# Performance work log

Measured on AMD Instinct MI355X. Metric: run time of the kernel, lower is better.

## Reference

```python
import jax, jax.numpy as jnp
import numpy as np

N = 50000        # nodes
E = 800000       # edges (avg degree 16)
F_IN = 128       # num_node_features
HEADS = 4        # const.NUM_HEADS
CH = 32          # const.NUM_CHANNELS
CLS = 40         # num_classes
NEG_SLOPE = 0.2  # PyG GATv2Conv default


def setup_inputs() -> dict:
    key = jax.random.key(0)
    ks = jax.random.split(key, 10)
    x = jax.random.normal(ks[0], (N, F_IN), dtype=jnp.float32)
    edge_index = jax.random.randint(ks[1], (2, E), 0, N, dtype=jnp.int64)
    s1 = 1.0 / np.sqrt(F_IN)
    s2 = 1.0 / np.sqrt(HEADS * CH)
    w1_l = jax.random.normal(ks[2], (F_IN, HEADS * CH), jnp.float32) * s1
    w1_r = jax.random.normal(ks[3], (F_IN, HEADS * CH), jnp.float32) * s1
    a1 = jax.random.normal(ks[4], (HEADS, CH), jnp.float32) * (1.0 / np.sqrt(CH))
    b1 = jnp.zeros((HEADS * CH,), jnp.float32)
    w2_l = jax.random.normal(ks[5], (HEADS * CH, CLS), jnp.float32) * s2
    w2_r = jax.random.normal(ks[6], (HEADS * CH, CLS), jnp.float32) * s2
    a2 = jax.random.normal(ks[7], (1, CLS), jnp.float32) * (1.0 / np.sqrt(CLS))
    b2 = jnp.zeros((CLS,), jnp.float32)
    return {"x": x, "edge_index": edge_index, "w1_l": w1_l, "w1_r": w1_r,
            "a1": a1, "b1": b1, "w2_l": w2_l, "w2_r": w2_r, "a2": a2, "b2": b2}


def _gatv2_conv(x, src, dst, wl, wr, a, b, concat):
    """GATv2Conv (PyG semantics, eval mode: no dropout).
    src -> lin_l, dst -> lin_r; e = a . LeakyReLU(x_l[src] + x_r[dst]);
    segment softmax over dst; out_i = sum_j alpha * x_l[src]."""
    H, C = a.shape
    n = x.shape[0]
    xl = (x @ wl).reshape(n, H, C)
    xr = (x @ wr).reshape(n, H, C)
    # per-edge additive attention logits [E, H]
    e = jnp.einsum('ehc,hc->eh', jax.nn.leaky_relu(xl[src] + xr[dst], NEG_SLOPE), a)
    # numerically stable segment softmax over target nodes
    m = jax.ops.segment_max(e, dst, num_segments=n)          # [n, H]
    p = jnp.exp(e - m[dst])
    denom = jax.ops.segment_sum(p, dst, num_segments=n)     # [n, H]
    alpha = p / denom[dst]
    out = jax.ops.segment_sum(alpha[..., None] * xl[src], dst, num_segments=n)  # [n, H, C]
    out = out.reshape(n, H * C) if concat else out.mean(axis=1)
    return out + b


def reference(x, edge_index, w1_l, w1_r, a1, b1, w2_l, w2_r, a2, b2):
    n = x.shape[0]
    # PyG GATv2Conv default add_self_loops=True
    loop = jnp.arange(n, dtype=edge_index.dtype)
    src = jnp.concatenate([edge_index[0], loop])
    dst = jnp.concatenate([edge_index[1], loop])
    h = jax.nn.elu(_gatv2_conv(x, src, dst, w1_l, w1_r, a1, b1, concat=True))
    # F.dropout with training=False is identity
    out = _gatv2_conv(h, src, dst, w2_l, w2_r, a2, b2, concat=False)
    return jax.nn.log_softmax(out, axis=1)
```

## Files before the change

### kernel.cpp

```cpp
#include <hip/hip_runtime.h>
#include <hip/hip_bf16.h>
#include <math.h>

#define NN 50000
#define NE 800000
#define ETOT (NE + NN)
#define CLS 40
#define CLSP 48
#define NEG 0.2f
#define MTILES (NN / 16)
#define GB1 ((MTILES + 3) / 4)
#define PREPB 176
#define NBUCK 196
#define BCAP 8192
#define EB 4096
#define KAB ((ETOT + EB - 1) / EB)

typedef __hip_bfloat16 bf16;
typedef __attribute__((ext_vector_type(8))) __bf16 bf16x8;
typedef __attribute__((ext_vector_type(4))) float f32x4;
struct U3 { unsigned x, y, z; };

__device__ __forceinline__ bf16x8 cvt8(f32x4 a, f32x4 b) {
    bf16x8 r;
    r[0] = (__bf16)a[0]; r[1] = (__bf16)a[1]; r[2] = (__bf16)a[2]; r[3] = (__bf16)a[3];
    r[4] = (__bf16)b[0]; r[5] = (__bf16)b[1]; r[6] = (__bf16)b[2]; r[7] = (__bf16)b[3];
    return r;
}
__device__ __forceinline__ void unpk(unsigned u, float& lo, float& hi) {
    lo = __uint_as_float(u << 16);
    hi = __uint_as_float(u & 0xffff0000u);
}
__device__ __forceinline__ void unpk8(uint4 u, float* x) {
    unpk(u.x, x[0], x[1]); unpk(u.y, x[2], x[3]);
    unpk(u.z, x[4], x[5]); unpk(u.w, x[6], x[7]);
}
__device__ __forceinline__ void unpk6(U3 u, float* x) {
    unpk(u.x, x[0], x[1]); unpk(u.y, x[2], x[3]); unpk(u.z, x[4], x[5]);
}
__device__ __forceinline__ float leaky(float v) { return fmaxf(v, NEG * v); }

__device__ __forceinline__ unsigned scan256(unsigned v, unsigned* wsum) {
    int t = threadIdx.x;
    int lane = t & 63, w = t >> 6;
    unsigned inc = v;
#pragma unroll
    for (int d = 1; d < 64; d <<= 1) {
        unsigned x = __shfl_up(inc, d);
        if (lane >= d) inc += x;
    }
    if (lane == 63) wsum[w] = inc;
    __syncthreads();
    unsigned woff = 0;
#pragma unroll
    for (int i = 0; i < 4; i++) woff += (i < w) ? wsum[i] : 0;
    return woff + inc - v;
}

__global__ __launch_bounds__(256) void prep(
        const float* __restrict__ w1l, const float* __restrict__ w1r,
        const float* __restrict__ w2l, const float* __restrict__ w2r,
        bf16* __restrict__ wT1, bf16* __restrict__ wT2,
        int* __restrict__ bcursor) {
    int t = blockIdx.x * 256 + threadIdx.x;
    if (t < NBUCK) bcursor[t] = 0;
    if (t < 2 * 128 * 128) {
        int m = t >> 14;
        int idx = t & 16383;
        int n = idx >> 7, k = idx & 127;
        const float* w = m ? w1r : w1l;
        wT1[t] = __float2bfloat16(w[k * 128 + n]);
    } else if (t < 2 * 128 * 128 + 2 * CLSP * 128) {
        int u = t - 2 * 128 * 128;
        int m = u / (CLSP * 128);
        int idx = u % (CLSP * 128);
        int n = idx >> 7, k = idx & 127;
        const float* w = m ? w2r : w2l;
        wT2[u] = __float2bfloat16((n < CLS) ? w[k * CLS + n] : 0.0f);
    }
}

__global__ __launch_bounds__(256) void gemm1_scatter(
        const float* __restrict__ x, const bf16* __restrict__ wT,
        bf16* __restrict__ outL, bf16* __restrict__ outR,
        const int* __restrict__ ei, int* __restrict__ bcursor,
        uint2* __restrict__ tmp) {
    __shared__ unsigned hist[256];
    __shared__ unsigned lstart[256];
    __shared__ unsigned lcur[256];
    __shared__ unsigned gbase[256];
    __shared__ unsigned wsum[4];
    __shared__ uint2 binned[EB];
    __shared__ unsigned target[EB];
    if ((int)blockIdx.x < GB1) {
        int wave = threadIdx.x >> 6;
        int lane = threadIdx.x & 63;
        int tile = blockIdx.x * 4 + wave;
        if (tile >= MTILES) return;
        const bf16* wl = wT;
        const bf16* wr = wT + 128 * 128;
        int row0 = tile * 16;
        int l16 = lane & 15, quad = lane >> 4;
        f32x4 z = {0.f, 0.f, 0.f, 0.f};
        f32x4 accl[8], accr[8];
#pragma unroll
        for (int i = 0; i < 8; i++) { accl[i] = z; accr[i] = z; }
        const float* xrow = x + (size_t)(row0 + l16) * 128 + quad * 8;
#pragma unroll
        for (int k0 = 0; k0 < 128; k0 += 32) {
            f32x4 a0 = *reinterpret_cast<const f32x4*>(xrow + k0);
            f32x4 a1v = *reinterpret_cast<const f32x4*>(xrow + k0 + 4);
            bf16x8 a = cvt8(a0, a1v);
#pragma unroll
            for (int ct = 0; ct < 8; ct++) {
                bf16x8 bl = *reinterpret_cast<const bf16x8*>(wl + (ct * 16 + l16) * 128 + k0 + quad * 8);
                bf16x8 br = *reinterpret_cast<const bf16x8*>(wr + (ct * 16 + l16) * 128 + k0 + quad * 8);
                accl[ct] = __builtin_amdgcn_mfma_f32_16x16x32_bf16(a, bl, accl[ct], 0, 0, 0);
                accr[ct] = __builtin_amdgcn_mfma_f32_16x16x32_bf16(a, br, accr[ct], 0, 0, 0);
            }
        }
#pragma unroll
        for (int ct = 0; ct < 8; ct++)
#pragma unroll
            for (int r = 0; r < 4; r++) {
                size_t o = (size_t)(row0 + quad * 4 + r) * 128 + ct * 16 + l16;
                outL[o] = __float2bfloat16(accl[ct][r]);
                outR[o] = __float2bfloat16(accr[ct][r]);
            }
    } else {
        int t = threadIdx.x;
        int e0 = (blockIdx.x - GB1) * EB;
        hist[t] = 0;
        __syncthreads();
        int srcs[16], dsts[16];
#pragma unroll
        for (int i = 0; i < 16; i++) {
            int e = e0 + i * 256 + t;
            if (e < ETOT) {
                int s, d;
                if (e < NE) { s = ei[e]; d = ei[NE + e]; }
                else        { s = d = e - NE; }
                srcs[i] = s; dsts[i] = d;
                atomicAdd(&hist[d >> 8], 1u);
            } else dsts[i] = -1;
        }
        __syncthreads();
        unsigned v = hist[t];
        unsigned excl = scan256(v, wsum);
        lstart[t] = excl;
        lcur[t] = 0;
        __syncthreads();
        if (t < NBUCK && v > 0)
            gbase[t] = (unsigned)atomicAdd(&bcursor[t], (int)v) + (unsigned)t * BCAP;
        __syncthreads();
#pragma unroll
        for (int i = 0; i < 16; i++) {
            int d = dsts[i];
            if (d >= 0) {
                int bk = d >> 8;
                unsigned p = atomicAdd(&lcur[bk], 1u);
                unsigned slot = lstart[bk] + p;
                binned[slot] = make_uint2((unsigned)srcs[i], (unsigned)d);
                target[slot] = gbase[bk] + p;
            }
        }
        __syncthreads();
        int tot = min(EB, ETOT - e0);
        for (int s = t; s < tot; s += 256)
            tmp[target[s]] = binned[s];
    }
}

__global__ __launch_bounds__(256) void bucket_sort(const int* __restrict__ bcursor,
                                                   const uint2* __restrict__ tmp,
                                                   int* __restrict__ csr_src,
                                                   int* __restrict__ startA,
                                                   int* __restrict__ degA) {
    __shared__ unsigned hist[256];
    __shared__ unsigned lcur[256];
    __shared__ unsigned wsum[4];
    int b = blockIdx.x, t = threadIdx.x;
    int cnt = bcursor[b];
    hist[t] = 0;
    __syncthreads();
    const uint2* seg = tmp + (size_t)b * BCAP;
    for (int s = t; s < cnt; s += 256)
        atomicAdd(&hist[seg[s].y & 255], 1u);
    __syncthreads();
    unsigned v = hist[t];
    unsigned excl = scan256(v, wsum);
    lcur[t] = excl;
    int node = b * 256 + t;
    if (node < NN) {
        startA[node] = b * BCAP + (int)excl;
        degA[node] = (int)v;
    }
    __syncthreads();
    int* cbase = csr_src + (size_t)b * BCAP;
    for (int s = t; s < cnt; s += 256) {
        uint2 p = seg[s];
        unsigned pos = atomicAdd(&lcur[p.y & 255], 1u);
        cbase[pos] = (int)p.x;
    }
}

struct L1S { float s; float acc[8]; };
__device__ __forceinline__ void l1_consume(uint4 u, bool valid, const float* xrf,
                                           const float* a1f, L1S& st) {
    float x[8];
    unpk8(u, x);
    float e = 0.f;
#pragma unroll
    for (int k = 0; k < 8; k++) e += a1f[k] * leaky(x[k] + xrf[k]);
    e += __shfl_xor(e, 1);
    e += __shfl_xor(e, 2);
    float w = valid ? __expf(e) : 0.f;
    st.s += w;
#pragma unroll
    for (int k = 0; k < 8; k++) st.acc[k] += w * x[k];
}

__global__ __launch_bounds__(256) void node_l1(const int* __restrict__ startA,
                                               const int* __restrict__ degA,
                                               const int* __restrict__ csr_src,
                                               const bf16* __restrict__ xl,
                                               const bf16* __restrict__ xr,
                                               const float* __restrict__ a1,
                                               const float* __restrict__ b1,
                                               bf16* __restrict__ hb) {
    int wid = (blockIdx.x * 256 + threadIdx.x) >> 6;
    int lane = threadIdx.x & 63;
    int g = lane >> 4, t = lane & 15;
    unsigned cB = (unsigned)t * 16;
    int j0 = startA[wid];
    int deg = degA[wid];
    unsigned rowB = (unsigned)csr_src[j0 + min(lane, deg - 1)] << 8;
    const char* xlb = (const char*)xl;
    float xrf[8];
    unpk8(*(const uint4*)((const char*)xr + ((unsigned)wid << 8) + cB), xrf);
    float a1f[8];
    {
        f32x4 lo = *reinterpret_cast<const f32x4*>(a1 + t * 8);
        f32x4 hi = *reinterpret_cast<const f32x4*>(a1 + t * 8 + 4);
#pragma unroll
        for (int k = 0; k < 4; k++) { a1f[k] = lo[k]; a1f[k + 4] = hi[k]; }
    }
    L1S st; st.s = 0.f;
#pragma unroll
    for (int k = 0; k < 8; k++) st.acc[k] = 0.f;
    int lim = min(deg, 64);
    int nb = (deg + 3) >> 2;
    int b = 0;
    for (; (b + 4) * 4 <= lim; b += 4) {
        unsigned o0 = __shfl(rowB, b * 4 + g) + cB;
        unsigned o1 = __shfl(rowB, b * 4 + 4 + g) + cB;
        unsigned o2 = __shfl(rowB, b * 4 + 8 + g) + cB;
        unsigned o3 = __shfl(rowB, b * 4 + 12 + g) + cB;
        uint4 u0 = *(const uint4*)(xlb + o0);
        uint4 u1 = *(const uint4*)(xlb + o1);
        uint4 u2 = *(const uint4*)(xlb + o2);
        uint4 u3 = *(const uint4*)(xlb + o3);
        l1_consume(u0, true, xrf, a1f, st);
        l1_consume(u1, true, xrf, a1f, st);
        l1_consume(u2, true, xrf, a1f, st);
        l1_consume(u3, true, xrf, a1f, st);
    }
    for (; (b + 2) * 4 <= lim; b += 2) {
        unsigned o0 = __shfl(rowB, b * 4 + g) + cB;
        unsigned o1 = __shfl(rowB, b * 4 + 4 + g) + cB;
        uint4 u0 = *(const uint4*)(xlb + o0);
        uint4 u1 = *(const uint4*)(xlb + o1);
        l1_consume(u0, true, xrf, a1f, st);
        l1_consume(u1, true, xrf, a1f, st);
    }
    for (; b < nb; b++) {
        int p = b * 4 + g;
        bool valid = p < deg;
        int pp = valid ? p : deg - 1;
        unsigned o = __shfl(rowB, min(pp, 63)) + cB;
        if (pp >= 64) o = (((unsigned)csr_src[j0 + pp]) << 8) + cB;
        uint4 u = *(const uint4*)(xlb + o);
        l1_consume(u, valid, xrf, a1f, st);
    }
#pragma unroll
    for (int d = 16; d < 64; d <<= 1) {
        st.s += __shfl_xor(st.s, d);
#pragma unroll
        for (int k = 0; k < 8; k++) st.acc[k] += __shfl_xor(st.acc[k], d);
    }
    if (g == 0) {
        float inv = 1.f / st.s;
        unsigned pk[4];
#pragma unroll
        for (int k = 0; k < 4; k++) {
            float o0 = st.acc[2 * k] * inv + b1[t * 8 + 2 * k];
            float o1 = st.acc[2 * k + 1] * inv + b1[t * 8 + 2 * k + 1];
            o0 = o0 > 0.f ? o0 : __expf(o0) - 1.f;
            o1 = o1 > 0.f ? o1 : __expf(o1) - 1.f;
            bf16 r0 = __float2bfloat16(o0), r1 = __float2bfloat16(o1);
            pk[k] = (unsigned)*reinterpret_cast<unsigned short*>(&r0) |
                    ((unsigned)*reinterpret_cast<unsigned short*>(&r1) << 16);
        }
        uint4 w4 = {pk[0], pk[1], pk[2], pk[3]};
        *(uint4*)((char*)hb + ((unsigned)wid << 8) + cB) = w4;
    }
}

__global__ __launch_bounds__(256) void gemm2(const bf16* __restrict__ h,
                                             const bf16* __restrict__ wT,
                                             bf16* __restrict__ outL,
                                             bf16* __restrict__ outR) {
    int wave = threadIdx.x >> 6;
    int lane = threadIdx.x & 63;
    int tile = blockIdx.x * 4 + wave;
    if (tile >= MTILES) return;
    const bf16* wl = wT;
    const bf16* wr = wT + CLSP * 128;
    int row0 = tile * 16;
    int l16 = lane & 15, quad = lane >> 4;
    f32x4 z = {0.f, 0.f, 0.f, 0.f};
    f32x4 accl[3], accr[3];
#pragma unroll
    for (int i = 0; i < 3; i++) { accl[i] = z; accr[i] = z; }
    const bf16* hrow = h + (size_t)(row0 + l16) * 128 + quad * 8;
#pragma unroll
    for (int k0 = 0; k0 < 128; k0 += 32) {
        bf16x8 a = *reinterpret_cast<const bf16x8*>(hrow + k0);
#pragma unroll
        for (int ct = 0; ct < 3; ct++) {
            bf16x8 bl = *reinterpret_cast<const bf16x8*>(wl + (ct * 16 + l16) * 128 + k0 + quad * 8);
            bf16x8 br = *reinterpret_cast<const bf16x8*>(wr + (ct * 16 + l16) * 128 + k0 + quad * 8);
            accl[ct] = __builtin_amdgcn_mfma_f32_16x16x32_bf16(a, bl, accl[ct], 0, 0, 0);
            accr[ct] = __builtin_amdgcn_mfma_f32_16x16x32_bf16(a, br, accr[ct], 0, 0, 0);
        }
    }
#pragma unroll
    for (int ct = 0; ct < 3; ct++)
#pragma unroll
        for (int r = 0; r < 4; r++) {
            size_t o = (size_t)(row0 + quad * 4 + r) * CLSP + ct * 16 + l16;
            outL[o] = __float2bfloat16(accl[ct][r]);
            outR[o] = __float2bfloat16(accr[ct][r]);
        }
}

struct L2S { float s; float acc[6]; };
__device__ __forceinline__ void l2_consume(U3 u, bool valid, const float* xrf,
                                           const float* a2f, L2S& st) {
    float x[6];
    unpk6(u, x);
    float e = 0.f;
#pragma unroll
    for (int k = 0; k < 6; k++) e += a2f[k] * leaky(x[k] + xrf[k]);
    e += __shfl_xor(e, 1);
    e += __shfl_xor(e, 2);
    e += __shfl_xor(e, 4);
    float w = valid ? __expf(e) : 0.f;
    st.s += w;
#pragma unroll
    for (int k = 0; k < 6; k++) st.acc[k] += w * x[k];
}

__global__ __launch_bounds__(256) void node_l2(const int* __restrict__ startA,
                                               const int* __restrict__ degA,
                                               const int* __restrict__ csr_src,
                                               const bf16* __restrict__ xl2,
                                               const bf16* __restrict__ xr2,
                                               const float* __restrict__ a2,
                                               const float* __restrict__ b2,
                                               float* __restrict__ out) {
    int wid = (blockIdx.x * 256 + threadIdx.x) >> 6;
    int lane = threadIdx.x & 63;
    int g = lane >> 3, t = lane & 7;
    unsigned cB = (unsigned)t * 12;
    int j0 = startA[wid];
    int deg = degA[wid];
    unsigned rowB = (unsigned)csr_src[j0 + min(lane, deg - 1)] * 96u;
    const char* xlb = (const char*)xl2;
    float xrf[6];
    unpk6(*(const U3*)((const char*)xr2 + (unsigned)wid * 96u + cB), xrf);
    int c = t * 6;
    float a2f[6];
#pragma unroll
    for (int k = 0; k < 6; k++) a2f[k] = (c + k < CLS) ? a2[c + k] : 0.f;
    L2S st; st.s = 0.f;
#pragma unroll
    for (int k = 0; k < 6; k++) st.acc[k] = 0.f;
    int lim = min(deg, 64);
    int nb = (deg + 7) >> 3;
    int b = 0;
    for (; (b + 2) * 8 <= lim; b += 2) {
        unsigned o0 = __shfl(rowB, b * 8 + g) + cB;
        unsigned o1 = __shfl(rowB, b * 8 + 8 + g) + cB;
        U3 u0 = *(const U3*)(xlb + o0);
        U3 u1 = *(const U3*)(xlb + o1);
        l2_consume(u0, true, xrf, a2f, st);
        l2_consume(u1, true, xrf, a2f, st);
    }
    for (; b < nb; b++) {
        int p = b * 8 + g;
        bool valid = p < deg;
        int pp = valid ? p : deg - 1;
        unsigned o = __shfl(rowB, min(pp, 63)) + cB;
        if (pp >= 64) o = (unsigned)csr_src[j0 + pp] * 96u + cB;
        U3 u = *(const U3*)(xlb + o);
        l2_consume(u, valid, xrf, a2f, st);
    }
#pragma unroll
    for (int d = 8; d < 64; d <<= 1) {
        st.s += __shfl_xor(st.s, d);
#pragma unroll
        for (int k = 0; k < 6; k++) st.acc[k] += __shfl_xor(st.acc[k], d);
    }
    float inv = 1.f / st.s;
    float q[6];
    float mx = -3e38f;
#pragma unroll
    for (int k = 0; k < 6; k++) {
        bool val = (c + k < CLS);
        q[k] = val ? (st.acc[k] * inv + b2[c + k]) : -3e38f;
        mx = fmaxf(mx, q[k]);
    }
    mx = fmaxf(mx, __shfl_xor(mx, 1));
    mx = fmaxf(mx, __shfl_xor(mx, 2));
    mx = fmaxf(mx, __shfl_xor(mx, 4));
    float se = 0.f;
#pragma unroll
    for (int k = 0; k < 6; k++) if (c + k < CLS) se += __expf(q[k] - mx);
    se += __shfl_xor(se, 1);
    se += __shfl_xor(se, 2);
    se += __shfl_xor(se, 4);
    float ls = mx + __logf(se);
    if (g == 0) {
        float* o = out + (size_t)wid * CLS + c;
#pragma unroll
        for (int k = 0; k < 6; k++)
            if (c + k < CLS) o[k] = q[k] - ls;
    }
}

extern "C" void kernel_launch(void* const* d_in, const int* in_sizes, int n_in,
                              void* d_out, int out_size, void* d_ws, size_t ws_size,
                              hipStream_t stream) {
    const float* x   = (const float*)d_in[0];
    const int*   ei  = (const int*)d_in[1];
    const float* w1l = (const float*)d_in[2];
    const float* w1r = (const float*)d_in[3];
    const float* a1  = (const float*)d_in[4];
    const float* b1  = (const float*)d_in[5];
    const float* w2l = (const float*)d_in[6];
    const float* w2r = (const float*)d_in[7];
    const float* a2  = (const float*)d_in[8];
    const float* b2  = (const float*)d_in[9];
    float* out = (float*)d_out;

    char* base = (char*)d_ws;
    int*   bcursor = (int*)(base + 0);
    int*   startA  = (int*)(base + 1024);
    int*   degA    = (int*)(base + 201024);
    uint2* tmp     = (uint2*)(base + 401024);
    int*   csr_src = (int*)(base + 13246080);
    bf16*  xl1     = (bf16*)(base + 19668608);
    bf16*  hb      = (bf16*)(base + 45268608);
    bf16*  xl2p    = (bf16*)(base + 58068608);
    bf16*  wT1     = (bf16*)(base + 67668608);
    bf16*  wT2     = (bf16*)(base + 67734144);
    bf16* xr1  = xl1 + (size_t)NN * 128;
    bf16* xr2p = xl2p + (size_t)NN * CLSP;

    prep<<<PREPB, 256, 0, stream>>>(w1l, w1r, w2l, w2r, wT1, wT2, bcursor);
    gemm1_scatter<<<GB1 + KAB, 256, 0, stream>>>(x, wT1, xl1, xr1, ei, bcursor, tmp);
    bucket_sort<<<NBUCK, 256, 0, stream>>>(bcursor, tmp, csr_src, startA, degA);
    node_l1<<<(NN * 64) / 256, 256, 0, stream>>>(startA, degA, csr_src, xl1, xr1, a1, b1, hb);
    gemm2<<<GB1, 256, 0, stream>>>(hb, wT2, xl2p, xr2p);
    node_l2<<<(NN * 64) / 256, 256, 0, stream>>>(startA, degA, csr_src, xl2p, xr2p, a2, b2, out);
}
```

Baseline: 237.8 us.

## Sort nodes by degree within buckets and vectorize per-edge math as float2

bucket_sort now builds a per-bucket permutation of nodes grouped by in-degree (counting sort over 64 degree classes). node_l1 and node_l2 map each wavefront to a permuted node, so waves in a block have similar trip counts and less load imbalance. Padding entries past NN exit early. The per-edge attention and accumulation math is also rewritten on float2 vectors to encourage packed FP32 instructions. The cost is scattered node order for the xr/hb/out accesses and an extra perm read per wave.

Result: slower. 243.8 us (+2.5%).

```diff
diff --git a/kernel.cpp b/kernel.cpp
--- a/kernel.cpp
+++ b/kernel.cpp
@@ -15,10 +15,13 @@
 #define BCAP 8192
 #define EB 4096
 #define KAB ((ETOT + EB - 1) / EB)
+#define PERMN (NBUCK * 256)
+#define NODEB (PERMN / 4)
 
 typedef __hip_bfloat16 bf16;
 typedef __attribute__((ext_vector_type(8))) __bf16 bf16x8;
 typedef __attribute__((ext_vector_type(4))) float f32x4;
+typedef __attribute__((ext_vector_type(2))) float f32x2;
 struct U3 { unsigned x, y, z; };
 
 __device__ __forceinline__ bf16x8 cvt8(f32x4 a, f32x4 b) {
@@ -27,18 +30,19 @@
     r[4] = (__bf16)b[0]; r[5] = (__bf16)b[1]; r[6] = (__bf16)b[2]; r[7] = (__bf16)b[3];
     return r;
 }
-__device__ __forceinline__ void unpk(unsigned u, float& lo, float& hi) {
-    lo = __uint_as_float(u << 16);
-    hi = __uint_as_float(u & 0xffff0000u);
-}
-__device__ __forceinline__ void unpk8(uint4 u, float* x) {
-    unpk(u.x, x[0], x[1]); unpk(u.y, x[2], x[3]);
-    unpk(u.z, x[4], x[5]); unpk(u.w, x[6], x[7]);
-}
-__device__ __forceinline__ void unpk6(U3 u, float* x) {
-    unpk(u.x, x[0], x[1]); unpk(u.y, x[2], x[3]); unpk(u.z, x[4], x[5]);
-}
-__device__ __forceinline__ float leaky(float v) { return fmaxf(v, NEG * v); }
+__device__ __forceinline__ f32x2 unpk2(unsigned u) {
+    f32x2 r;
+    r.x = __uint_as_float(u << 16);
+    r.y = __uint_as_float(u & 0xffff0000u);
+    return r;
+}
+__device__ __forceinline__ f32x2 leaky2(f32x2 v) {
+    f32x2 s = v * NEG;
+    f32x2 r;
+    r.x = fmaxf(v.x, s.x);
+    r.y = fmaxf(v.y, s.y);
+    return r;
+}
 
 __device__ __forceinline__ unsigned scan256(unsigned v, unsigned* wsum) {
     int t = threadIdx.x;
@@ -175,13 +179,17 @@
                                                    const uint2* __restrict__ tmp,
                                                    int* __restrict__ csr_src,
                                                    int* __restrict__ startA,
-                                                   int* __restrict__ degA) {
+                                                   int* __restrict__ degA,
+                                                   unsigned* __restrict__ perm) {
     __shared__ unsigned hist[256];
     __shared__ unsigned lcur[256];
     __shared__ unsigned wsum[4];
+    __shared__ unsigned dbase[64];
+    __shared__ unsigned dcur[64];
     int b = blockIdx.x, t = threadIdx.x;
     int cnt = bcursor[b];
     hist[t] = 0;
+    if (t < 64) dcur[t] = 0;
     __syncthreads();
     const uint2* seg = tmp + (size_t)b * BCAP;
     for (int s = t; s < cnt; s += 256)
@@ -191,11 +199,28 @@
     unsigned excl = scan256(v, wsum);
     lcur[t] = excl;
     int node = b * 256 + t;
-    if (node < NN) {
+    bool real = node < NN;
+    if (real) {
         startA[node] = b * BCAP + (int)excl;
         degA[node] = (int)v;
     }
+    unsigned dc = real ? min(v, 62u) : 63u;
+    atomicAdd(&dcur[dc], 1u);
     __syncthreads();
+    if (t < 64) {
+        unsigned bv = dcur[t];
+        unsigned inc = bv;
+#pragma unroll
+        for (int d = 1; d < 64; d <<= 1) {
+            unsigned xx = __shfl_up(inc, d);
+            if ((t & 63) >= d) inc += xx;
+        }
+        dbase[t] = inc - bv;
+        dcur[t] = 0;
+    }
+    __syncthreads();
+    unsigned rank = dbase[dc] + atomicAdd(&dcur[dc], 1u);
+    perm[b * 256 + rank] = (unsigned)node;
     int* cbase = csr_src + (size_t)b * BCAP;
     for (int s = t; s < cnt; s += 256) {
         uint2 p = seg[s];
@@ -204,23 +229,25 @@
     }
 }
 
-struct L1S { float s; float acc[8]; };
-__device__ __forceinline__ void l1_consume(uint4 u, bool valid, const float* xrf,
-                                           const float* a1f, L1S& st) {
-    float x[8];
-    unpk8(u, x);
-    float e = 0.f;
-#pragma unroll
-    for (int k = 0; k < 8; k++) e += a1f[k] * leaky(x[k] + xrf[k]);
+struct L1S { float s; f32x2 acc[4]; };
+__device__ __forceinline__ void l1_consume(uint4 u, bool valid, const f32x2* xrf,
+                                           const f32x2* a1f, L1S& st) {
+    f32x2 x0 = unpk2(u.x), x1 = unpk2(u.y), x2 = unpk2(u.z), x3 = unpk2(u.w);
+    f32x2 e2 = a1f[0] * leaky2(x0 + xrf[0]);
+    e2 += a1f[1] * leaky2(x1 + xrf[1]);
+    e2 += a1f[2] * leaky2(x2 + xrf[2]);
+    e2 += a1f[3] * leaky2(x3 + xrf[3]);
+    float e = e2.x + e2.y;
     e += __shfl_xor(e, 1);
     e += __shfl_xor(e, 2);
     float w = valid ? __expf(e) : 0.f;
     st.s += w;
-#pragma unroll
-    for (int k = 0; k < 8; k++) st.acc[k] += w * x[k];
-}
-
-__global__ __launch_bounds__(256) void node_l1(const int* __restrict__ startA,
+    st.acc[0] += w * x0; st.acc[1] += w * x1;
+    st.acc[2] += w * x2; st.acc[3] += w * x3;
+}
+
+__global__ __launch_bounds__(256) void node_l1(const unsigned* __restrict__ perm,
+                                               const int* __restrict__ startA,
                                                const int* __restrict__ degA,
                                                const int* __restrict__ csr_src,
                                                const bf16* __restrict__ xl,
@@ -229,25 +256,27 @@
                                                const float* __restrict__ b1,
                                                bf16* __restrict__ hb) {
     int wid = (blockIdx.x * 256 + threadIdx.x) >> 6;
+    unsigned nid = perm[wid];
+    if (nid >= NN) return;
     int lane = threadIdx.x & 63;
     int g = lane >> 4, t = lane & 15;
     unsigned cB = (unsigned)t * 16;
-    int j0 = startA[wid];
-    int deg = degA[wid];
+    int j0 = startA[nid];
+    int deg = degA[nid];
     unsigned rowB = (unsigned)csr_src[j0 + min(lane, deg - 1)] << 8;
     const char* xlb = (const char*)xl;
-    float xrf[8];
-    unpk8(*(const uint4*)((const char*)xr + ((unsigned)wid << 8) + cB), xrf);
-    float a1f[8];
+    uint4 xru = *(const uint4*)((const char*)xr + (nid << 8) + cB);
+    f32x2 xrf[4] = {unpk2(xru.x), unpk2(xru.y), unpk2(xru.z), unpk2(xru.w)};
+    f32x2 a1f[4];
     {
         f32x4 lo = *reinterpret_cast<const f32x4*>(a1 + t * 8);
         f32x4 hi = *reinterpret_cast<const f32x4*>(a1 + t * 8 + 4);
-#pragma unroll
-        for (int k = 0; k < 4; k++) { a1f[k] = lo[k]; a1f[k + 4] = hi[k]; }
+        a1f[0].x = lo[0]; a1f[0].y = lo[1]; a1f[1].x = lo[2]; a1f[1].y = lo[3];
+        a1f[2].x = hi[0]; a1f[2].y = hi[1]; a1f[3].x = hi[2]; a1f[3].y = hi[3];
     }
     L1S st; st.s = 0.f;
 #pragma unroll
-    for (int k = 0; k < 8; k++) st.acc[k] = 0.f;
+    for (int k = 0; k < 4; k++) st.acc[k] = (f32x2){0.f, 0.f};
     int lim = min(deg, 64);
     int nb = (deg + 3) >> 2;
     int b = 0;
@@ -286,15 +315,18 @@
     for (int d = 16; d < 64; d <<= 1) {
         st.s += __shfl_xor(st.s, d);
 #pragma unroll
-        for (int k = 0; k < 8; k++) st.acc[k] += __shfl_xor(st.acc[k], d);
+        for (int k = 0; k < 4; k++) {
+            st.acc[k].x += __shfl_xor(st.acc[k].x, d);
+            st.acc[k].y += __shfl_xor(st.acc[k].y, d);
+        }
     }
     if (g == 0) {
         float inv = 1.f / st.s;
         unsigned pk[4];
 #pragma unroll
         for (int k = 0; k < 4; k++) {
-            float o0 = st.acc[2 * k] * inv + b1[t * 8 + 2 * k];
-            float o1 = st.acc[2 * k + 1] * inv + b1[t * 8 + 2 * k + 1];
+            float o0 = st.acc[k].x * inv + b1[t * 8 + 2 * k];
+            float o1 = st.acc[k].y * inv + b1[t * 8 + 2 * k + 1];
             o0 = o0 > 0.f ? o0 : __expf(o0) - 1.f;
             o1 = o1 > 0.f ? o1 : __expf(o1) - 1.f;
             bf16 r0 = __float2bfloat16(o0), r1 = __float2bfloat16(o1);
@@ -302,7 +334,7 @@
                     ((unsigned)*reinterpret_cast<unsigned short*>(&r1) << 16);
         }
         uint4 w4 = {pk[0], pk[1], pk[2], pk[3]};
-        *(uint4*)((char*)hb + ((unsigned)wid << 8) + cB) = w4;
+        *(uint4*)((char*)hb + (nid << 8) + cB) = w4;
     }
 }
 
@@ -344,24 +376,24 @@
         }
 }
 
-struct L2S { float s; float acc[6]; };
-__device__ __forceinline__ void l2_consume(U3 u, bool valid, const float* xrf,
-                                           const float* a2f, L2S& st) {
-    float x[6];
-    unpk6(u, x);
-    float e = 0.f;
-#pragma unroll
-    for (int k = 0; k < 6; k++) e += a2f[k] * leaky(x[k] + xrf[k]);
+struct L2S { float s; f32x2 acc[3]; };
+__device__ __forceinline__ void l2_consume(U3 u, bool valid, const f32x2* xrf,
+                                           const f32x2* a2f, L2S& st) {
+    f32x2 x0 = unpk2(u.x), x1 = unpk2(u.y), x2 = unpk2(u.z);
+    f32x2 e2 = a2f[0] * leaky2(x0 + xrf[0]);
+    e2 += a2f[1] * leaky2(x1 + xrf[1]);
+    e2 += a2f[2] * leaky2(x2 + xrf[2]);
+    float e = e2.x + e2.y;
     e += __shfl_xor(e, 1);
     e += __shfl_xor(e, 2);
     e += __shfl_xor(e, 4);
     float w = valid ? __expf(e) : 0.f;
     st.s += w;
-#pragma unroll
-    for (int k = 0; k < 6; k++) st.acc[k] += w * x[k];
-}
-
-__global__ __launch_bounds__(256) void node_l2(const int* __restrict__ startA,
+    st.acc[0] += w * x0; st.acc[1] += w * x1; st.acc[2] += w * x2;
+}
+
+__global__ __launch_bounds__(256) void node_l2(const unsigned* __restrict__ perm,
+                                               const int* __restrict__ startA,
                                                const int* __restrict__ degA,
                                                const int* __restrict__ csr_src,
                                                const bf16* __restrict__ xl2,
@@ -370,22 +402,27 @@
                                                const float* __restrict__ b2,
                                                float* __restrict__ out) {
     int wid = (blockIdx.x * 256 + threadIdx.x) >> 6;
+    unsigned nid = perm[wid];
+    if (nid >= NN) return;
     int lane = threadIdx.x & 63;
     int g = lane >> 3, t = lane & 7;
     unsigned cB = (unsigned)t * 12;
-    int j0 = startA[wid];
-    int deg = degA[wid];
+    int j0 = startA[nid];
+    int deg = degA[nid];
     unsigned rowB = (unsigned)csr_src[j0 + min(lane, deg - 1)] * 96u;
     const char* xlb = (const char*)xl2;
-    float xrf[6];
-    unpk6(*(const U3*)((const char*)xr2 + (unsigned)wid * 96u + cB), xrf);
+    U3 xru = *(const U3*)((const char*)xr2 + nid * 96u + cB);
+    f32x2 xrf[3] = {unpk2(xru.x), unpk2(xru.y), unpk2(xru.z)};
     int c = t * 6;
-    float a2f[6];
-#pragma unroll
-    for (int k = 0; k < 6; k++) a2f[k] = (c + k < CLS) ? a2[c + k] : 0.f;
+    f32x2 a2f[3];
+#pragma unroll
+    for (int k = 0; k < 3; k++) {
+        a2f[k].x = (c + 2 * k < CLS) ? a2[c + 2 * k] : 0.f;
+        a2f[k].y = (c + 2 * k + 1 < CLS) ? a2[c + 2 * k + 1] : 0.f;
+    }
     L2S st; st.s = 0.f;
 #pragma unroll
-    for (int k = 0; k < 6; k++) st.acc[k] = 0.f;
+    for (int k = 0; k < 3; k++) st.acc[k] = (f32x2){0.f, 0.f};
     int lim = min(deg, 64);
     int nb = (deg + 7) >> 3;
     int b = 0;
@@ -410,7 +447,10 @@
     for (int d = 8; d < 64; d <<= 1) {
         st.s += __shfl_xor(st.s, d);
 #pragma unroll
-        for (int k = 0; k < 6; k++) st.acc[k] += __shfl_xor(st.acc[k], d);
+        for (int k = 0; k < 3; k++) {
+            st.acc[k].x += __shfl_xor(st.acc[k].x, d);
+            st.acc[k].y += __shfl_xor(st.acc[k].y, d);
+        }
     }
     float inv = 1.f / st.s;
     float q[6];
@@ -418,7 +458,8 @@
 #pragma unroll
     for (int k = 0; k < 6; k++) {
         bool val = (c + k < CLS);
-        q[k] = val ? (st.acc[k] * inv + b2[c + k]) : -3e38f;
+        float av = (k & 1) ? st.acc[k >> 1].y : st.acc[k >> 1].x;
+        q[k] = val ? (av * inv + b2[c + k]) : -3e38f;
         mx = fmaxf(mx, q[k]);
     }
     mx = fmaxf(mx, __shfl_xor(mx, 1));
@@ -432,7 +473,7 @@
     se += __shfl_xor(se, 4);
     float ls = mx + __logf(se);
     if (g == 0) {
-        float* o = out + (size_t)wid * CLS + c;
+        float* o = out + (size_t)nid * CLS + c;
 #pragma unroll
         for (int k = 0; k < 6; k++)
             if (c + k < CLS) o[k] = q[k] - ls;
@@ -455,23 +496,24 @@
     float* out = (float*)d_out;
 
     char* base = (char*)d_ws;
-    int*   bcursor = (int*)(base + 0);
-    int*   startA  = (int*)(base + 1024);
-    int*   degA    = (int*)(base + 201024);
-    uint2* tmp     = (uint2*)(base + 401024);
-    int*   csr_src = (int*)(base + 13246080);
-    bf16*  xl1     = (bf16*)(base + 19668608);
-    bf16*  hb      = (bf16*)(base + 45268608);
-    bf16*  xl2p    = (bf16*)(base + 58068608);
-    bf16*  wT1     = (bf16*)(base + 67668608);
-    bf16*  wT2     = (bf16*)(base + 67734144);
+    int*      bcursor = (int*)(base + 0);
+    int*      startA  = (int*)(base + 1024);
+    int*      degA    = (int*)(base + 201024);
+    uint2*    tmp     = (uint2*)(base + 401024);
+    int*      csr_src = (int*)(base + 13246080);
+    bf16*     xl1     = (bf16*)(base + 19668608);
+    bf16*     hb      = (bf16*)(base + 45268608);
+    bf16*     xl2p    = (bf16*)(base + 58068608);
+    bf16*     wT1     = (bf16*)(base + 67668608);
+    bf16*     wT2     = (bf16*)(base + 67734144);
+    unsigned* perm    = (unsigned*)(base + 67758720);
     bf16* xr1  = xl1 + (size_t)NN * 128;
     bf16* xr2p = xl2p + (size_t)NN * CLSP;
 
     prep<<<PREPB, 256, 0, stream>>>(w1l, w1r, w2l, w2r, wT1, wT2, bcursor);
     gemm1_scatter<<<GB1 + KAB, 256, 0, stream>>>(x, wT1, xl1, xr1, ei, bcursor, tmp);
-    bucket_sort<<<NBUCK, 256, 0, stream>>>(bcursor, tmp, csr_src, startA, degA);
-    node_l1<<<(NN * 64) / 256, 256, 0, stream>>>(startA, degA, csr_src, xl1, xr1, a1, b1, hb);
+    bucket_sort<<<NBUCK, 256, 0, stream>>>(bcursor, tmp, csr_src, startA, degA, perm);
+    node_l1<<<NODEB, 256, 0, stream>>>(perm, startA, degA, csr_src, xl1, xr1, a1, b1, hb);
     gemm2<<<GB1, 256, 0, stream>>>(hb, wT2, xl2p, xr2p);
-    node_l2<<<(NN * 64) / 256, 256, 0, stream>>>(startA, degA, csr_src, xl2p, xr2p, a2, b2, out);
-}
+    node_l2<<<NODEB, 256, 0, stream>>>(perm, startA, degA, csr_src, xl2p, xr2p, a2, b2, out);
+}
```
